# Kernel optimization log

Measured on AMD Instinct MI355X. Metric: run time of the kernel, lower is better.

Reference implementation:

```python
import jax, jax.numpy as jnp
import numpy as np

SQRT_2_OVER_PI = float(np.sqrt(2.0 / np.pi))
EPS = 1e-5
EPS_VAR = 1e-4
NORM_EPS = 1e-12  # F.normalize default


def _gelu_tanh(x):
    return 0.5 * x * (1.0 + jnp.tanh(SQRT_2_OVER_PI * (x + 0.044715 * x ** 3)))


def setup_inputs() -> dict:
    key = jax.random.key(0)
    k1, k2, k3, k4 = jax.random.split(key, 4)
    B, T, D = 4, 4096, 2048
    x = jax.random.normal(k1, (B, T, D), dtype=jnp.float32)
    ema_mean = 0.1 * jax.random.normal(k2, (D,), dtype=jnp.float32)
    # ensure ema_sq - ema_mean^2 > 0 so variance clamp is realistic
    ema_sq = ema_mean ** 2 + jax.random.uniform(k3, (D,), dtype=jnp.float32, minval=0.5, maxval=1.5)
    ema_out = jax.random.normal(k4, (D,), dtype=jnp.float32)
    return {
        "x": x,
        "ema_mean": ema_mean,
        "ema_sq": ema_sq,
        "ema_out": ema_out,
        "surp_ema": jnp.float32(0.05),
        "log_tau": jnp.float32(np.log(2.0)),
        "log_sigma": jnp.float32(np.log(np.exp(0.3) - 1.0)),
        "log_w_raw": jnp.float32(np.log(np.exp(1.0) - 1.0)),
    }


def reference(x, ema_mean, ema_sq, ema_out, surp_ema, log_tau, log_sigma, log_w_raw):
    # learned scalar transforms (differentiable)
    tau = jnp.exp(log_tau)
    sigma = jax.nn.softplus(log_sigma)
    w = jax.nn.softplus(log_w_raw)

    out = _gelu_tanh(x)  # [B,T,D]

    # --- surprise score: z-score vs EMA stats (all detached in torch) ---
    xd = jax.lax.stop_gradient(x)
    mu = jax.lax.stop_gradient(ema_mean)                     # [D]
    var = jnp.maximum(jax.lax.stop_gradient(ema_sq) - mu ** 2, EPS_VAR)
    std = jnp.sqrt(var)                                      # [D]
    z = (xd - mu) / (std + EPS)                               # [B,T,D]
    mean_absz = jnp.mean(jnp.abs(z), axis=-1)                 # [B,T]

    surp_raw = jnp.tanh(sigma * mean_absz)                    # grad flows only via sigma
    surp_mod = jax.nn.relu(surp_raw - jax.lax.stop_gradient(surp_ema))

    # --- cosine similarity of detached output vs EMA direction ---
    outd = jax.lax.stop_gradient(out)
    out_n = outd / jnp.maximum(jnp.linalg.norm(outd, axis=-1, keepdims=True), NORM_EPS)
    eo = jax.lax.stop_gradient(ema_out)
    ema_n = eo / jnp.maximum(jnp.linalg.norm(eo), NORM_EPS)   # [D]
    cos_sim = jnp.clip(jnp.sum(out_n * ema_n, axis=-1), -1.0, 1.0)  # [B,T]

    gate = jnp.exp(-tau * cos_sim) * (1.0 + w * surp_mod)     # [B,T]
    return out * gate[..., None]
```

## Files before the change

kernel.cpp:

```cpp
#include <hip/hip_runtime.h>
#include <math.h>

#define D 2048
#define NT 256
#define ROWS_PER_BLOCK 4
#define V_PER_LANE 8

typedef float floatx4 __attribute__((ext_vector_type(4)));

__global__ __launch_bounds__(NT) void fused_gate_kernel(
    const float* __restrict__ x,
    const float* __restrict__ ema_mean,
    const float* __restrict__ ema_sq,
    const float* __restrict__ ema_out,
    const float* __restrict__ surp_ema,
    const float* __restrict__ log_tau,
    const float* __restrict__ log_sigma,
    const float* __restrict__ log_w_raw,
    float* __restrict__ out) {
  const int t = threadIdx.x;
  const int lane = t & 63;
  const int wave = t >> 6;
  const int row = blockIdx.x * ROWS_PER_BLOCK + wave;

  const float* __restrict__ xr = x + (size_t)row * D;
  float* __restrict__ outr = out + (size_t)row * D;

  const float tau    = __expf(log_tau[0]);
  const float sigma  = log1pf(__expf(log_sigma[0]));
  const float w      = log1pf(__expf(log_w_raw[0]));
  const float surp_e = surp_ema[0];

  const float c1 = -2.0f * 0.7978845608028654f;
  const float c2 = c1 * 0.044715f;

  float o[V_PER_LANE * 4];
  float s_absz = 0.f, s_o2 = 0.f, s_dot = 0.f, s_e2 = 0.f;

#pragma unroll
  for (int i = 0; i < V_PER_LANE; ++i) {
    const int v = lane + i * 64;
    const floatx4 xv = __builtin_nontemporal_load((const floatx4*)xr + v);
    const floatx4 mv = ((const floatx4*)ema_mean)[v];
    const floatx4 qv = ((const floatx4*)ema_sq)[v];
    const floatx4 ev = ((const floatx4*)ema_out)[v];
#pragma unroll
    for (int j = 0; j < 4; ++j) {
      const float xx = xv[j];
      const float x2 = xx * xx;
      const float u2 = xx * fmaf(c2, x2, c1);
      const float g  = xx * __builtin_amdgcn_rcpf(1.0f + __expf(u2));
      o[i * 4 + j] = g;
      const float mu  = mv[j];
      const float var = fmaxf(fmaf(-mu, mu, qv[j]), 1e-4f);
      const float inv = __builtin_amdgcn_rsqf(var);
      s_absz += fabsf((xx - mu) * inv);
      const float e = ev[j];
      s_o2  = fmaf(g, g, s_o2);
      s_dot = fmaf(g, e, s_dot);
      s_e2  = fmaf(e, e, s_e2);
    }
  }

#pragma unroll
  for (int off = 32; off > 0; off >>= 1) {
    s_absz += __shfl_xor(s_absz, off);
    s_o2   += __shfl_xor(s_o2, off);
    s_dot  += __shfl_xor(s_dot, off);
    s_e2   += __shfl_xor(s_e2, off);
  }

  const float mean_absz = s_absz * (1.0f / (float)D);
  const float surp_raw  = tanhf(sigma * mean_absz);
  const float surp_mod  = fmaxf(surp_raw - surp_e, 0.0f);
  const float inv_no = __builtin_amdgcn_rsqf(fmaxf(s_o2, 1e-24f));
  const float inv_ne = __builtin_amdgcn_rsqf(fmaxf(s_e2, 1e-24f));
  float cs = s_dot * inv_no * inv_ne;
  cs = fminf(fmaxf(cs, -1.0f), 1.0f);
  const float gate = __expf(-tau * cs) * (1.0f + w * surp_mod);

#pragma unroll
  for (int i = 0; i < V_PER_LANE; ++i) {
    const int v = lane + i * 64;
    floatx4 r;
    r[0] = o[i * 4 + 0] * gate;
    r[1] = o[i * 4 + 1] * gate;
    r[2] = o[i * 4 + 2] * gate;
    r[3] = o[i * 4 + 3] * gate;
    __builtin_nontemporal_store(r, (floatx4*)outr + v);
  }
}

extern "C" void kernel_launch(void* const* d_in, const int* in_sizes, int n_in,
                              void* d_out, int out_size, void* d_ws, size_t ws_size,
                              hipStream_t stream) {
  const float* x        = (const float*)d_in[0];
  const float* ema_mean = (const float*)d_in[1];
  const float* ema_sq   = (const float*)d_in[2];
  const float* ema_out  = (const float*)d_in[3];
  const float* surp_ema = (const float*)d_in[4];
  const float* log_tau  = (const float*)d_in[5];
  const float* log_sig  = (const float*)d_in[6];
  const float* log_wr   = (const float*)d_in[7];
  float* out = (float*)d_out;

  const int rows = in_sizes[0] / D;
  fused_gate_kernel<<<rows / ROWS_PER_BLOCK, NT, 0, stream>>>(
      x, ema_mean, ema_sq, ema_out, surp_ema, log_tau, log_sig, log_wr, out);
}
```

Measured before the change: 242.5 us.

## Precompute per-column EMA stats in shared memory and use larger blocks

Each block now precomputes inverse std, mean times inverse std, and the ema_out values for all columns once into LDS. The per-element loop reads them from shared memory instead of reloading three global vectors and redoing the rsqrt for every row. The block grows to 8 rows and 512 threads to amortize the precompute, and the x load drops its nontemporal hint. This costs 24KB of LDS and a barrier per block, which may limit occupancy and delay the first x loads.

```diff
diff --git a/kernel.cpp b/kernel.cpp
--- a/kernel.cpp
+++ b/kernel.cpp
@@ -2,9 +2,10 @@
 #include <math.h>
 
 #define D 2048
-#define NT 256
-#define ROWS_PER_BLOCK 4
+#define NT 512
+#define ROWS_PER_BLOCK 8
 #define V_PER_LANE 8
+#define V4 (D / 4)
 
 typedef float floatx4 __attribute__((ext_vector_type(4)));
 
@@ -18,10 +19,32 @@
     const float* __restrict__ log_sigma,
     const float* __restrict__ log_w_raw,
     float* __restrict__ out) {
+  __shared__ floatx4 s_inv[V4];
+  __shared__ floatx4 s_mui[V4];
+  __shared__ floatx4 s_e[V4];
+
   const int t = threadIdx.x;
   const int lane = t & 63;
   const int wave = t >> 6;
   const int row = blockIdx.x * ROWS_PER_BLOCK + wave;
+
+  {
+    const floatx4 mv = ((const floatx4*)ema_mean)[t];
+    const floatx4 qv = ((const floatx4*)ema_sq)[t];
+    const floatx4 ev = ((const floatx4*)ema_out)[t];
+    floatx4 iv, miv;
+#pragma unroll
+    for (int j = 0; j < 4; ++j) {
+      const float mu  = mv[j];
+      const float var = fmaxf(fmaf(-mu, mu, qv[j]), 1e-4f);
+      iv[j]  = __builtin_amdgcn_rsqf(var);
+      miv[j] = mu * iv[j];
+    }
+    s_inv[t] = iv;
+    s_mui[t] = miv;
+    s_e[t]   = ev;
+  }
+  __syncthreads();
 
   const float* __restrict__ xr = x + (size_t)row * D;
   float* __restrict__ outr = out + (size_t)row * D;
@@ -40,10 +63,10 @@
 #pragma unroll
   for (int i = 0; i < V_PER_LANE; ++i) {
     const int v = lane + i * 64;
-    const floatx4 xv = __builtin_nontemporal_load((const floatx4*)xr + v);
-    const floatx4 mv = ((const floatx4*)ema_mean)[v];
-    const floatx4 qv = ((const floatx4*)ema_sq)[v];
-    const floatx4 ev = ((const floatx4*)ema_out)[v];
+    const floatx4 xv  = ((const floatx4*)xr)[v];
+    const floatx4 iv  = s_inv[v];
+    const floatx4 miv = s_mui[v];
+    const floatx4 ev  = s_e[v];
 #pragma unroll
     for (int j = 0; j < 4; ++j) {
       const float xx = xv[j];
@@ -51,10 +74,7 @@
       const float u2 = xx * fmaf(c2, x2, c1);
       const float g  = xx * __builtin_amdgcn_rcpf(1.0f + __expf(u2));
       o[i * 4 + j] = g;
-      const float mu  = mv[j];
-      const float var = fmaxf(fmaf(-mu, mu, qv[j]), 1e-4f);
-      const float inv = __builtin_amdgcn_rsqf(var);
-      s_absz += fabsf((xx - mu) * inv);
+      s_absz += fabsf(fmaf(xx, iv[j], -miv[j]));
       const float e = ev[j];
       s_o2  = fmaf(g, g, s_o2);
       s_dot = fmaf(g, e, s_dot);
```

New measurement: 249.6 us. +2.9%, slower.
